# Kernel optimization log

Hardware: AMD Instinct MI355X
Metric: run time of the kernel (lower is better)

The kernel has to match this reference:

```python
import jax, jax.numpy as jnp
import numpy as np

M = 23          # number of dendritic subunits
N_SYN = 1500    # number of synapses
T = 30000       # timesteps
B = 101         # temporal kernel length (odd -> 'same' output length)
G_NO = 4        # synapse groups (first half excitatory double-exp kernel)
PAD = B // 2
# parent (1-based) of each subunit; 0 marks root; children have higher index
C_DEN = np.array([0] + [((m - 1) // 2) + 1 for m in range(1, M)], dtype=np.int64)
G_ASSIGN = np.arange(N_SYN, dtype=np.int64) % G_NO   # synapse -> group
SYN_SUB = np.arange(N_SYN, dtype=np.int64) % M       # synapse -> subunit (C_syn nonzeros)


def setup_inputs() -> dict:
    key = jax.random.key(0)
    X = jax.random.uniform(key, (T, N_SYN), dtype=jnp.float32)
    V_o = jnp.ones((1,), jnp.float32) * -69.0
    Tau = jnp.ones((G_NO,), jnp.float32) * 1.4
    Delta = jnp.ones((1,), jnp.float32) * 0.25
    W = jnp.concatenate([jnp.full((G_NO // 2,), 2.0, jnp.float32),
                         jnp.full((G_NO - G_NO // 2,), -1.0, jnp.float32)]) * 0.05
    C = jnp.ones((M,), jnp.float32)
    Theta = jnp.zeros((M,), jnp.float32)
    return {"X": X, "V_o": V_o, "Tau": Tau, "Delta": Delta, "W": W, "C": C, "Theta": Theta}


def _group_kernels(Tau, Delta):
    # shared shifted time base, clamped at 0
    t = jnp.maximum(jnp.arange(B, dtype=jnp.float32) - jnp.exp(Delta[0]), 0.0)  # [B]
    tau = jnp.exp(Tau)[:, None]                               # [G_NO, 1]
    tf = t[None, :] / tau
    fast = tf * jnp.exp(-tf)                                   # alpha kernel
    ts = t[None, :] / (tau * 2.8 + 10.4)
    slow = ts * jnp.exp(-ts) * 0.3
    exc = (fast + slow) / 1.3                                  # dual-exp for excitatory groups
    is_exc = (jnp.arange(G_NO) < G_NO // 2)[:, None]
    return jnp.where(is_exc, exc, fast)                        # [G_NO, B]


def _forward(X, V_o, Tau, Delta, W, C, Theta):
    kern = _group_kernels(Tau, Delta)                          # [G_NO, B]
    g = jnp.asarray(G_ASSIGN)
    # conv is linear, so fold the per-group weight W[g] into the kernel
    k_syn = kern[g] * W[g][:, None]                            # [N_SYN, B]
    # depthwise cross-correlation (matches torch F.conv1d), 'same' padding
    filt = jax.lax.conv_general_dilated(
        X.T[None],                 # [1, N, T]
        k_syn[:, None, :],         # [N, 1, B]
        window_strides=(1,), padding=[(PAD, PAD)],
        feature_group_count=N_SYN,
        dimension_numbers=('NCH', 'OIH', 'NCH'))[0].T          # [T, N]
    # gather-sum of synapses into subunits (C_syn sign only selects membership)
    A = jax.nn.one_hot(jnp.asarray(SYN_SUB), M, dtype=X.dtype)  # [N, M]
    sub_in = filt @ A                                           # [T, M]
    expC = jnp.exp(C)
    # internal nodes processed from leaves toward root (descending indices)
    roots = (np.flip(np.unique(C_DEN))[:-1] - 1).astype(int)
    root_set = set(roots.tolist())
    out = [None] * M
    for m in range(M):                                          # leaves
        if m not in root_set:
            out[m] = jax.nn.sigmoid(sub_in[:, m] - Theta[m]) * expC[m]
    for r in roots:                                             # tree reduction
        s = sub_in[:, r]
        for k in np.where(C_DEN == r + 1)[0]:
            s = s + out[k]
        out[r] = jax.nn.sigmoid(s - Theta[r]) * expC[r]
    return out[0] + V_o[0]                                      # [T]


def reference(X, V_o, Tau, Delta, W, C, Theta):
    return _forward(X, V_o, Tau, Delta, W, C, Theta)
```

## Files before the change

kernel.cpp:

```cpp
#include <hip/hip_runtime.h>
#include <cstddef>

#define T_DIM 30000
#define M_DIM 23
#define NJ    92
#define TILE  64
#define STR   184
#define SUBS  25
#define XP4   377

typedef short bf16x8 __attribute__((ext_vector_type(8)));
typedef float f32x4  __attribute__((ext_vector_type(4)));

__device__ __forceinline__ unsigned short f2bf(float f) {
    unsigned int u = __float_as_uint(f);
    return (unsigned short)((u + 0x7fffu + ((u >> 16) & 1u)) >> 16);
}

__global__ __launch_bounds__(128) void reduce_k(const float* __restrict__ X,
                                                const float* __restrict__ Tau,
                                                const float* __restrict__ Delta,
                                                const float* __restrict__ W,
                                                unsigned short* __restrict__ Yb,
                                                unsigned int* __restrict__ afrag) {
    __shared__ __align__(16) float4 Xs[2 * XP4];

    const int tid = threadIdx.x;
    const int tb  = blockIdx.x * 2;

    const float4* Xg = reinterpret_cast<const float4*>(X) + (size_t)tb * 375;
    #pragma unroll
    for (int it = 0; it < 6; ++it) {
        int i = tid + 128 * it;
        if (i < 750) {
            int r = (i >= 375) ? 1 : 0;
            int pos = i - r * 375;
            Xs[r * XP4 + pos] = Xg[i];
        }
    }
    __syncthreads();

    if (tid < 46) {
        int r = tid / 23;
        int q = tid - 23 * r;
        const float4* row = &Xs[r * XP4];
        float4 s = make_float4(0.f, 0.f, 0.f, 0.f);
        #pragma unroll
        for (int k = 0; k < 16; ++k) {
            float4 v = row[q + 23 * k];
            s.x += v.x; s.y += v.y; s.z += v.z; s.w += v.w;
        }
        if (q < 7) {
            float4 v = row[q + 23 * 16];
            s.x += v.x; s.y += v.y; s.z += v.z; s.w += v.w;
        }
        ushort4 o;
        o.x = f2bf(s.x); o.y = f2bf(s.y); o.z = f2bf(s.z); o.w = f2bf(s.w);
        reinterpret_cast<ushort4*>(Yb)[(size_t)(tb + r) * 23 + q] = o;
    }

    if (blockIdx.x == 0) {
        for (int item = tid; item < 1024; item += 128) {
            int f = item >> 6;
            int l = item & 63;
            int g = f >> 2, kk = f & 3;
            float eD  = __expf(Delta[0]);
            float tau = __expf(Tau[g]);
            float wg  = W[g];
            unsigned short vals[8];
            #pragma unroll
            for (int j = 0; j < 8; ++j) {
                int x = kk * 32 + ((l >> 4) << 3) + j - (l & 15);
                float val = 0.f;
                if (x >= 0 && x <= 100) {
                    float tt  = fmaxf((float)x - eD, 0.f);
                    float tf  = tt / tau;
                    float fast = tf * __expf(-tf);
                    float kv;
                    if (g < 2) {
                        float ts = tt / (tau * 2.8f + 10.4f);
                        kv = (fast + ts * __expf(-ts) * 0.3f) * (1.0f / 1.3f);
                    } else {
                        kv = fast;
                    }
                    val = kv * wg;
                }
                vals[j] = f2bf(val);
            }
            uint4 o;
            o.x = (unsigned)vals[0] | ((unsigned)vals[1] << 16);
            o.y = (unsigned)vals[2] | ((unsigned)vals[3] << 16);
            o.z = (unsigned)vals[4] | ((unsigned)vals[5] << 16);
            o.w = (unsigned)vals[6] | ((unsigned)vals[7] << 16);
            reinterpret_cast<uint4*>(afrag)[f * 64 + l] = o;
        }
    }
}

__global__ __launch_bounds__(512, 4) void conv_tree_k(
    const unsigned short* __restrict__ Yb,
    const unsigned int* __restrict__ afrag,
    const float* __restrict__ Vo,
    const float* __restrict__ C,
    const float* __restrict__ Theta,
    float* __restrict__ out)
{
    __shared__ __align__(16) unsigned short Yt[NJ * STR];
    __shared__ float sub[TILE * SUBS];
    __shared__ float sTheta[M_DIM];
    __shared__ float sExpC[M_DIM];

    const int tid = threadIdx.x;
    const int t0  = blockIdx.x * TILE;

    if (tid < M_DIM) {
        sTheta[tid] = Theta[tid];
        sExpC[tid]  = __expf(C[tid]);
    }

    {
        unsigned int* Yw = reinterpret_cast<unsigned int*>(Yt);
        for (int i = tid; i < 88 * 23; i += 512) {
            int rp = i / 23;
            int q  = i - rp * 23;
            int g0 = t0 - 50 + 2 * rp;
            ushort4 ra = make_ushort4(0, 0, 0, 0);
            ushort4 rb = make_ushort4(0, 0, 0, 0);
            if ((unsigned)g0       < (unsigned)T_DIM) ra = reinterpret_cast<const ushort4*>(Yb)[(size_t)g0 * 23 + q];
            if ((unsigned)(g0 + 1) < (unsigned)T_DIM) rb = reinterpret_cast<const ushort4*>(Yb)[(size_t)(g0 + 1) * 23 + q];
            Yw[(q     ) * 92 + rp] = (unsigned)ra.x | ((unsigned)rb.x << 16);
            Yw[(q + 23) * 92 + rp] = (unsigned)ra.y | ((unsigned)rb.y << 16);
            Yw[(q + 46) * 92 + rp] = (unsigned)ra.z | ((unsigned)rb.z << 16);
            Yw[(q + 69) * 92 + rp] = (unsigned)ra.w | ((unsigned)rb.w << 16);
        }
    }

    const int l    = tid & 63;
    const int wave = tid >> 6;
    const int dt   = (wave & 3) * 16;
    const int nt   = wave >> 2;
    const int n    = l & 15;
    const int m    = nt * 16 + n;
    const bool mvalid = (m < M_DIM);
    const int mc   = mvalid ? m : 0;
    const int kq   = (l >> 4) << 3;

    __syncthreads();

    f32x4 acc = {0.f, 0.f, 0.f, 0.f};
    const uint4* AF = reinterpret_cast<const uint4*>(afrag);

    #pragma unroll
    for (int g = 0; g < 4; ++g) {
        int a  = (3 * ((g - mc) & 3)) & 3;
        int j  = mc + 23 * a;
        int cp = (j >> 2) + 23 * g;
        const unsigned short* colp = &Yt[cp * STR + dt + kq];

        uint4 a0 = AF[(g * 4 + 0) * 64 + l];
        uint4 a1 = AF[(g * 4 + 1) * 64 + l];
        uint4 a2 = AF[(g * 4 + 2) * 64 + l];
        uint4 a3 = AF[(g * 4 + 3) * 64 + l];

        bf16x8 b0 = *reinterpret_cast<const bf16x8*>(colp);
        acc = __builtin_amdgcn_mfma_f32_16x16x32_bf16(__builtin_bit_cast(bf16x8, a0), b0, acc, 0, 0, 0);
        bf16x8 b1 = *reinterpret_cast<const bf16x8*>(colp + 32);
        acc = __builtin_amdgcn_mfma_f32_16x16x32_bf16(__builtin_bit_cast(bf16x8, a1), b1, acc, 0, 0, 0);
        bf16x8 b2 = *reinterpret_cast<const bf16x8*>(colp + 64);
        acc = __builtin_amdgcn_mfma_f32_16x16x32_bf16(__builtin_bit_cast(bf16x8, a2), b2, acc, 0, 0, 0);
        bf16x8 b3 = *reinterpret_cast<const bf16x8*>(colp + 96);
        acc = __builtin_amdgcn_mfma_f32_16x16x32_bf16(__builtin_bit_cast(bf16x8, a3), b3, acc, 0, 0, 0);
    }

    if (mvalid) {
        int i0 = (l >> 4) * 4;
        #pragma unroll
        for (int r = 0; r < 4; ++r)
            sub[(dt + i0 + r) * SUBS + m] = acc[r];
    }
    __syncthreads();

    if (tid < TILE) {
        int t = t0 + tid;
        if (t < T_DIM) {
            const float* s = &sub[tid * SUBS];
            float o[M_DIM];
            #pragma unroll
            for (int mm = 11; mm < 23; ++mm) {
                float x = s[mm] - sTheta[mm];
                o[mm] = sExpC[mm] / (1.f + __expf(-x));
            }
            #pragma unroll
            for (int rr = 10; rr >= 0; --rr) {
                float x = s[rr] + o[2 * rr + 1] + o[2 * rr + 2] - sTheta[rr];
                o[rr] = sExpC[rr] / (1.f + __expf(-x));
            }
            out[t] = o[0] + Vo[0];
        }
    }
}

extern "C" void kernel_launch(void* const* d_in, const int* in_sizes, int n_in,
                              void* d_out, int out_size, void* d_ws, size_t ws_size,
                              hipStream_t stream) {
    const float* X     = (const float*)d_in[0];
    const float* Vo    = (const float*)d_in[1];
    const float* Tau   = (const float*)d_in[2];
    const float* Delta = (const float*)d_in[3];
    const float* W     = (const float*)d_in[4];
    const float* C     = (const float*)d_in[5];
    const float* Theta = (const float*)d_in[6];
    float* out = (float*)d_out;

    unsigned short* Yb  = (unsigned short*)d_ws;
    unsigned int* afrag = (unsigned int*)((char*)d_ws + (size_t)T_DIM * NJ * 2);

    reduce_k<<<T_DIM / 2, 128, 0, stream>>>(X, Tau, Delta, W, Yb, afrag);
    conv_tree_k<<<(T_DIM + TILE - 1) / TILE, 512, 0, stream>>>(
        Yb, afrag, Vo, C, Theta, out);
}
```

Baseline: 38.34 us.

## Store reduced inputs column-major with zero padding, read MFMA operands from global

The reduction kernel now transposes its bf16 per-column sums through shared memory and writes them into a column-major, zero-padded global buffer. Block indices are swizzled so that concurrently running blocks write to spread-out time positions. The conv kernel drops its shared-memory staging, the transpose and the barrier, and loads MFMA B operands straight from that padded global layout. This trades LDS staging and a sync for scattered 4-byte global writes and unstaged global reads, which rely on caching for reuse across the overlapping time windows.

```diff
diff --git a/kernel.cpp b/kernel.cpp
--- a/kernel.cpp
+++ b/kernel.cpp
@@ -5,9 +5,11 @@
 #define M_DIM 23
 #define NJ    92
 #define TILE  64
-#define STR   184
 #define SUBS  25
 #define XP4   377
+#define PADC  50
+#define CSTR  30208
+#define CSTR32 (CSTR/2)
 
 typedef short bf16x8 __attribute__((ext_vector_type(8)));
 typedef float f32x4  __attribute__((ext_vector_type(4)));
@@ -17,16 +19,19 @@
     return (unsigned short)((u + 0x7fffu + ((u >> 16) & 1u)) >> 16);
 }
 
-__global__ __launch_bounds__(128) void reduce_k(const float* __restrict__ X,
+__global__ __launch_bounds__(128) void reduce_t(const float* __restrict__ X,
                                                 const float* __restrict__ Tau,
                                                 const float* __restrict__ Delta,
                                                 const float* __restrict__ W,
-                                                unsigned short* __restrict__ Yb,
+                                                unsigned short* __restrict__ Ycp,
                                                 unsigned int* __restrict__ afrag) {
     __shared__ __align__(16) float4 Xs[2 * XP4];
+    __shared__ unsigned short Ytr[92 * 2];
 
     const int tid = threadIdx.x;
-    const int tb  = blockIdx.x * 2;
+    const int b   = blockIdx.x;
+    const int swb = (b & 7) * 1875 + (b >> 3);
+    const int tb  = swb * 2;
 
     const float4* Xg = reinterpret_cast<const float4*>(X) + (size_t)tb * 375;
     #pragma unroll
@@ -54,12 +59,25 @@
             float4 v = row[q + 23 * 16];
             s.x += v.x; s.y += v.y; s.z += v.z; s.w += v.w;
         }
-        ushort4 o;
-        o.x = f2bf(s.x); o.y = f2bf(s.y); o.z = f2bf(s.z); o.w = f2bf(s.w);
-        reinterpret_cast<ushort4*>(Yb)[(size_t)(tb + r) * 23 + q] = o;
-    }
-
-    if (blockIdx.x == 0) {
+        Ytr[(4 * q + 0) * 2 + r] = f2bf(s.x);
+        Ytr[(4 * q + 1) * 2 + r] = f2bf(s.y);
+        Ytr[(4 * q + 2) * 2 + r] = f2bf(s.z);
+        Ytr[(4 * q + 3) * 2 + r] = f2bf(s.w);
+    }
+    __syncthreads();
+
+    if (tid < 92) {
+        unsigned int v = (unsigned)Ytr[tid * 2] | ((unsigned)Ytr[tid * 2 + 1] << 16);
+        reinterpret_cast<unsigned int*>(Ycp)[(size_t)tid * CSTR32 + (PADC + tb) / 2] = v;
+    }
+
+    if (b < 92 && tid < 104) {
+        unsigned int* col32 = reinterpret_cast<unsigned int*>(Ycp) + (size_t)b * CSTR32;
+        int u = (tid < 25) ? tid : (15025 + (tid - 25));
+        col32[u] = 0u;
+    }
+
+    if (b == 0) {
         for (int item = tid; item < 1024; item += 128) {
             int f = item >> 6;
             int l = item & 63;
@@ -98,44 +116,26 @@
 }
 
 __global__ __launch_bounds__(512, 4) void conv_tree_k(
-    const unsigned short* __restrict__ Yb,
+    const unsigned short* __restrict__ Ycp,
     const unsigned int* __restrict__ afrag,
     const float* __restrict__ Vo,
     const float* __restrict__ C,
     const float* __restrict__ Theta,
     float* __restrict__ out)
 {
-    __shared__ __align__(16) unsigned short Yt[NJ * STR];
     __shared__ float sub[TILE * SUBS];
     __shared__ float sTheta[M_DIM];
     __shared__ float sExpC[M_DIM];
 
     const int tid = threadIdx.x;
     const int t0  = blockIdx.x * TILE;
+    const int l   = tid & 63;
 
     if (tid < M_DIM) {
         sTheta[tid] = Theta[tid];
         sExpC[tid]  = __expf(C[tid]);
     }
 
-    {
-        unsigned int* Yw = reinterpret_cast<unsigned int*>(Yt);
-        for (int i = tid; i < 88 * 23; i += 512) {
-            int rp = i / 23;
-            int q  = i - rp * 23;
-            int g0 = t0 - 50 + 2 * rp;
-            ushort4 ra = make_ushort4(0, 0, 0, 0);
-            ushort4 rb = make_ushort4(0, 0, 0, 0);
-            if ((unsigned)g0       < (unsigned)T_DIM) ra = reinterpret_cast<const ushort4*>(Yb)[(size_t)g0 * 23 + q];
-            if ((unsigned)(g0 + 1) < (unsigned)T_DIM) rb = reinterpret_cast<const ushort4*>(Yb)[(size_t)(g0 + 1) * 23 + q];
-            Yw[(q     ) * 92 + rp] = (unsigned)ra.x | ((unsigned)rb.x << 16);
-            Yw[(q + 23) * 92 + rp] = (unsigned)ra.y | ((unsigned)rb.y << 16);
-            Yw[(q + 46) * 92 + rp] = (unsigned)ra.z | ((unsigned)rb.z << 16);
-            Yw[(q + 69) * 92 + rp] = (unsigned)ra.w | ((unsigned)rb.w << 16);
-        }
-    }
-
-    const int l    = tid & 63;
     const int wave = tid >> 6;
     const int dt   = (wave & 3) * 16;
     const int nt   = wave >> 2;
@@ -145,17 +145,14 @@
     const int mc   = mvalid ? m : 0;
     const int kq   = (l >> 4) << 3;
 
-    __syncthreads();
+    const uint4* AF = reinterpret_cast<const uint4*>(afrag);
 
     f32x4 acc = {0.f, 0.f, 0.f, 0.f};
-    const uint4* AF = reinterpret_cast<const uint4*>(afrag);
-
     #pragma unroll
     for (int g = 0; g < 4; ++g) {
         int a  = (3 * ((g - mc) & 3)) & 3;
         int j  = mc + 23 * a;
-        int cp = (j >> 2) + 23 * g;
-        const unsigned short* colp = &Yt[cp * STR + dt + kq];
+        const unsigned short* colp = Ycp + (size_t)j * CSTR + t0 + dt + kq;
 
         uint4 a0 = AF[(g * 4 + 0) * 64 + l];
         uint4 a1 = AF[(g * 4 + 1) * 64 + l];
@@ -212,10 +209,9 @@
     const float* Theta = (const float*)d_in[6];
     float* out = (float*)d_out;
 
-    unsigned short* Yb  = (unsigned short*)d_ws;
-    unsigned int* afrag = (unsigned int*)((char*)d_ws + (size_t)T_DIM * NJ * 2);
-
-    reduce_k<<<T_DIM / 2, 128, 0, stream>>>(X, Tau, Delta, W, Yb, afrag);
-    conv_tree_k<<<(T_DIM + TILE - 1) / TILE, 512, 0, stream>>>(
-        Yb, afrag, Vo, C, Theta, out);
-}
+    unsigned short* Ycp = (unsigned short*)d_ws;
+    unsigned int* afrag = (unsigned int*)((char*)d_ws + (size_t)NJ * CSTR * 2);
+
+    reduce_t<<<T_DIM / 2, 128, 0, stream>>>(X, Tau, Delta, W, Ycp, afrag);
+    conv_tree_k<<<469, 512, 0, stream>>>(Ycp, afrag, Vo, C, Theta, out);
+}
```

Result: slower. 43.28 us (+12.9%).
